# Optimization experiments

Measured on AMD Instinct MI355X. Metric: run time of the kernel, lower is better.

Reference implementation:

```python
import jax, jax.numpy as jnp
import numpy as np


def setup_inputs() -> dict:
    key = jax.random.key(0)
    ks = jax.random.split(key, 8)
    B, C, W, H = 4, 256, 64, 64
    Ck = C // 8  # 32, key/query channels
    x = jax.random.normal(ks[0], (B, C, W, H), dtype=jnp.float32)
    # 1x1 conv weights (xavier-uniform-like scale), biases zero per init_conv
    sf = (6.0 / (C + Ck)) ** 0.5
    sh = (6.0 / (C + C)) ** 0.5
    Wf = jax.random.uniform(ks[1], (Ck, C), jnp.float32, -sf, sf)
    Wg = jax.random.uniform(ks[2], (Ck, C), jnp.float32, -sf, sf)
    Wh = jax.random.uniform(ks[3], (C, C), jnp.float32, -sh, sh)
    bf = jnp.zeros((Ck,), jnp.float32)
    bg = jnp.zeros((Ck,), jnp.float32)
    bh = jnp.zeros((C,), jnp.float32)
    gamma = jax.random.uniform(ks[4], (1,), jnp.float32) * 0.5
    return {"x": x, "Wf": Wf, "bf": bf, "Wg": Wg, "bg": bg,
            "Wh": Wh, "bh": bh, "gamma": gamma}


def reference(x, Wf, bf, Wg, bg, Wh, bh, gamma):
    B, C, W, H = x.shape
    N = W * H
    xf = x.reshape(B, C, N)  # [B, C, N]
    # 1x1 convs == per-pixel linear maps
    f = jnp.einsum('kc,bcn->bkn', Wf, xf) + bf[None, :, None]  # [B, C/8, N]
    g = jnp.einsum('kc,bcn->bkn', Wg, xf) + bg[None, :, None]  # [B, C/8, N]
    h = jnp.einsum('oc,bcn->bon', Wh, xf) + bh[None, :, None]  # [B, C,   N]
    # attention[b, i, j] = sum_k f[b,k,i] * g[b,k,j]; softmax over j
    attn = jax.nn.softmax(jnp.einsum('bki,bkj->bij', f, g), axis=-1)  # [B,N,N]
    # bmm(h, attention): out[b,c,i] = sum_j h[b,c,j] * attn[b,j,i]
    sa = jnp.einsum('bcj,bji->bci', h, attn).reshape(B, C, W, H)
    return gamma[0] * sa + x
```

## Files before the change

### kernel.cpp

```cpp
#include <hip/hip_runtime.h>

#define NB 4
#define NC 256
#define NCK 32
#define NPIX 4096
#define TOT (NB * NC * NPIX)

typedef unsigned short u16;
typedef unsigned int u32;
typedef __bf16 bfv8 __attribute__((ext_vector_type(8)));
typedef float f32x4 __attribute__((ext_vector_type(4)));
#define LOG2E 1.4426950408889634f

__device__ inline u16 f2bf(float f) {
  union { float f; u32 u; } v; v.f = f;
  u32 r = v.u + 0x7fffu + ((v.u >> 16) & 1u);
  return (u16)(r >> 16);
}
__device__ inline float bf2f(u16 h) {
  union { u32 u; float f; } v; v.u = (u32)h << 16; return v.f;
}
__device__ inline u32 cvtpk(float a, float b) {
  u32 r;
  asm("v_cvt_pk_bf16_f32 %0, %1, %2" : "=v"(r) : "v"(a), "v"(b));
  return r;
}

__global__ __launch_bounds__(256) void k_fg(const float* __restrict__ x,
                                            const float* __restrict__ Wf,
                                            const float* __restrict__ bf_,
                                            const float* __restrict__ Wg,
                                            const float* __restrict__ bg_,
                                            u16* __restrict__ fP,
                                            u16* __restrict__ gT,
                                            u16* __restrict__ xT) {
  __shared__ float Wt[256][65];
  __shared__ float xl[32][68];
  __shared__ float tb[64][68];
  int blk = blockIdx.x;
  int b = blk >> 6;
  int n0 = (blk & 63) * 64;
  int t = threadIdx.x;
  int tx = t & 15, ty = t >> 4;
  for (int r = 0; r < 64; r++) {
    float w = (r < 32) ? Wf[r * 256 + t] : Wg[(r - 32) * 256 + t];
    Wt[t][r] = w;
  }
  float acc[4][4] = {};
  int n = t >> 2, cp = t & 3;
  for (int kc = 0; kc < 8; kc++) {
    __syncthreads();
#pragma unroll
    for (int r = 0; r < 2; r++) {
      int e = (r * 256 + t) * 4;
      int row = e >> 6, col = e & 63;
      *(float4*)&xl[row][col] =
          *(const float4*)(x + ((size_t)(b * NC + kc * 32 + row)) * NPIX + n0 + col);
    }
    __syncthreads();
    {
      u32 uu[4];
#pragma unroll
      for (int q = 0; q < 4; q++)
        uu[q] = cvtpk(xl[cp * 8 + 2 * q][n], xl[cp * 8 + 2 * q + 1][n]);
      *(uint4*)(xT + ((size_t)(b * NPIX) + n0 + n) * NC + kc * 32 + cp * 8) =
          make_uint4(uu[0], uu[1], uu[2], uu[3]);
    }
#pragma unroll
    for (int kk = 0; kk < 32; kk++) {
      float4 xv = *(const float4*)&xl[kk][tx * 4];
      float w0 = Wt[kc * 32 + kk][ty * 4 + 0];
      float w1 = Wt[kc * 32 + kk][ty * 4 + 1];
      float w2 = Wt[kc * 32 + kk][ty * 4 + 2];
      float w3 = Wt[kc * 32 + kk][ty * 4 + 3];
      acc[0][0] += w0 * xv.x; acc[0][1] += w0 * xv.y; acc[0][2] += w0 * xv.z; acc[0][3] += w0 * xv.w;
      acc[1][0] += w1 * xv.x; acc[1][1] += w1 * xv.y; acc[1][2] += w1 * xv.z; acc[1][3] += w1 * xv.w;
      acc[2][0] += w2 * xv.x; acc[2][1] += w2 * xv.y; acc[2][2] += w2 * xv.z; acc[2][3] += w2 * xv.w;
      acc[3][0] += w3 * xv.x; acc[3][1] += w3 * xv.y; acc[3][2] += w3 * xv.z; acc[3][3] += w3 * xv.w;
    }
  }
#pragma unroll
  for (int j = 0; j < 4; j++) {
    int o = ty * 4 + j;
    float bias = (o < 32) ? bf_[o] : bg_[o - 32];
#pragma unroll
    for (int vi = 0; vi < 4; vi++) tb[tx * 4 + vi][o] = acc[j][vi] + bias;
  }
  __syncthreads();
  int part = t & 3;
  {
    u32 ph[4], plo[4];
#pragma unroll
    for (int e = 0; e < 4; e++) {
      float v0 = tb[n][part * 8 + 2 * e + 0];
      float v1 = tb[n][part * 8 + 2 * e + 1];
      u16 h0 = f2bf(v0), h1 = f2bf(v1);
      u16 l0 = f2bf(v0 - bf2f(h0)), l1 = f2bf(v1 - bf2f(h1));
      ph[e] = (u32)h0 | ((u32)h1 << 16);
      plo[e] = (u32)l0 | ((u32)l1 << 16);
    }
    int jt_g = (n0 >> 4) + (n >> 4), r = n & 15;
    u16* dst = fP + ((size_t)(b * 256) + jt_g) * 1024 + r * 32 + part * 8;
    *(uint4*)dst = make_uint4(ph[0], ph[1], ph[2], ph[3]);
    *(uint4*)(dst + 512) = make_uint4(plo[0], plo[1], plo[2], plo[3]);
  }
  {
    u32 ph[4], plo[4];
#pragma unroll
    for (int e = 0; e < 4; e++) {
      float v0 = tb[n][32 + part * 8 + 2 * e + 0];
      float v1 = tb[n][32 + part * 8 + 2 * e + 1];
      u16 h0 = f2bf(v0), h1 = f2bf(v1);
      u16 l0 = f2bf(v0 - bf2f(h0)), l1 = f2bf(v1 - bf2f(h1));
      ph[e] = (u32)h0 | ((u32)h1 << 16);
      plo[e] = (u32)l0 | ((u32)l1 << 16);
    }
    u16* dst = gT + ((size_t)(b * NPIX) + n0 + n) * 64 + part * 8;
    *(uint4*)dst = make_uint4(ph[0], ph[1], ph[2], ph[3]);
    *(uint4*)(dst + 32) = make_uint4(plo[0], plo[1], plo[2], plo[3]);
  }
}

__global__ __launch_bounds__(256) void k_h(const u16* __restrict__ xT,
                                           const float* __restrict__ Wh,
                                           const float* __restrict__ bh,
                                           u16* __restrict__ h2) {
  __shared__ u16 At[128 * 32];
  __shared__ u16 Bt[128 * 32];
  int blk = blockIdx.x;
  int b = blk >> 6, r = blk & 63;
  int nt = r >> 1, ot = r & 1;
  int n0 = nt * 128, o0 = ot * 128;
  int t = threadIdx.x, lane = t & 63, w = t >> 6;
  int wr = w >> 1, wc = w & 1;
  int coll = lane & 15, cg = lane >> 4;
  f32x4 acc[4][4] = {};
  for (int kc = 0; kc < 8; kc++) {
    __syncthreads();
#pragma unroll
    for (int r2 = 0; r2 < 2; r2++) {
      int s = r2 * 256 + t;
      int row = s >> 2, slot = s & 3;
      int sw = (row ^ (row >> 2)) & 3;
      uint4 va = *(const uint4*)(xT + ((size_t)(b * NPIX + n0 + row)) * NC + kc * 32 + slot * 8);
      *(uint4*)((char*)At + row * 64 + ((slot ^ sw) * 16)) = va;
      const float* wsrc = Wh + (size_t)(o0 + row) * NC + kc * 32 + slot * 8;
      float4 w0 = *(const float4*)wsrc;
      float4 w1 = *(const float4*)(wsrc + 4);
      uint4 vb = make_uint4(cvtpk(w0.x, w0.y), cvtpk(w0.z, w0.w),
                            cvtpk(w1.x, w1.y), cvtpk(w1.z, w1.w));
      *(uint4*)((char*)Bt + row * 64 + ((slot ^ sw) * 16)) = vb;
    }
    __syncthreads();
    bfv8 af[4], bfr[4];
#pragma unroll
    for (int mi = 0; mi < 4; mi++) {
      int row = wr * 64 + mi * 16 + coll;
      int slot = cg ^ ((row ^ (row >> 2)) & 3);
      af[mi] = *(const bfv8*)((const char*)At + row * 64 + slot * 16);
    }
#pragma unroll
    for (int ni = 0; ni < 4; ni++) {
      int row = wc * 64 + ni * 16 + coll;
      int slot = cg ^ ((row ^ (row >> 2)) & 3);
      bfr[ni] = *(const bfv8*)((const char*)Bt + row * 64 + slot * 16);
    }
#pragma unroll
    for (int mi = 0; mi < 4; mi++)
#pragma unroll
      for (int ni = 0; ni < 4; ni++)
        acc[mi][ni] = __builtin_amdgcn_mfma_f32_16x16x32_bf16(af[mi], bfr[ni], acc[mi][ni], 0, 0, 0);
  }
#pragma unroll
  for (int ni = 0; ni < 4; ni++) {
    int o = o0 + wc * 64 + ni * 16 + coll;
    float bias = bh[o];
#pragma unroll
    for (int mi = 0; mi < 4; mi++) {
      int px = n0 + wr * 64 + mi * 16 + cg * 4;
      u32 lo = cvtpk(acc[mi][ni][0] + bias, acc[mi][ni][1] + bias);
      u32 hi = cvtpk(acc[mi][ni][2] + bias, acc[mi][ni][3] + bias);
      *(uint2*)(h2 + (((size_t)(b * 128) + (px >> 5)) * NC + o) * 32 + (px & 31)) =
          make_uint2(lo, hi);
    }
  }
}

__global__ __launch_bounds__(256) void k_pass1(const u16* __restrict__ fP,
                                               const u16* __restrict__ gT,
                                               float2* __restrict__ pmd) {
  __shared__ u16 gs[64 * 64];
  int blk = blockIdx.x;
  int iq = blk & 7, jt = (blk >> 3) & 63, b = blk >> 9;
  int j0 = jt * 64, ibase = iq * 512;
  int t = threadIdx.x, lane = t & 63, w = t >> 6;
  int coll = lane & 15, cg = lane >> 4;
  const u16* fr = fP + ((size_t)(b * 256) + (j0 >> 4) + w) * 1024 + coll * 32 + cg * 8;
  bfv8 ah = *(const bfv8*)fr;
  bfv8 al = *(const bfv8*)(fr + 512);
  float m[4] = {-3e38f, -3e38f, -3e38f, -3e38f}, d[4] = {0.f, 0.f, 0.f, 0.f};
  int r0 = t >> 3, s0 = t & 7;
  uint4 v0 = *(const uint4*)(gT + ((size_t)(b * NPIX) + ibase + r0) * 64 + s0 * 8);
  uint4 v1 = *(const uint4*)(gT + ((size_t)(b * NPIX) + ibase + 32 + r0) * 64 + s0 * 8);
  for (int it2 = 0; it2 < 8; ++it2) {
    __syncthreads();
    *(uint4*)(&gs[r0 * 64 + ((s0 ^ (r0 & 7)) << 3)]) = v0;
    *(uint4*)(&gs[(32 + r0) * 64 + ((s0 ^ (r0 & 7)) << 3)]) = v1;
    __syncthreads();
    if (it2 < 7) {
      v0 = *(const uint4*)(gT + ((size_t)(b * NPIX) + ibase + (it2 + 1) * 64 + r0) * 64 + s0 * 8);
      v1 = *(const uint4*)(gT + ((size_t)(b * NPIX) + ibase + (it2 + 1) * 64 + 32 + r0) * 64 + s0 * 8);
    }
    float sv[4][4];
#pragma unroll
    for (int t4 = 0; t4 < 4; ++t4) {
      int row = t4 * 16 + coll;
      const u16* base = &gs[row * 64];
      bfv8 bh = *(const bfv8*)(base + ((cg ^ (row & 7)) << 3));
      bfv8 bl = *(const bfv8*)(base + (((4 + cg) ^ (row & 7)) << 3));
      f32x4 s = {0.f, 0.f, 0.f, 0.f};
      s = __builtin_amdgcn_mfma_f32_16x16x32_bf16(al, bh, s, 0, 0, 0);
      s = __builtin_amdgcn_mfma_f32_16x16x32_bf16(ah, bl, s, 0, 0, 0);
      s = __builtin_amdgcn_mfma_f32_16x16x32_bf16(ah, bh, s, 0, 0, 0);
      sv[t4][0] = s[0]; sv[t4][1] = s[1]; sv[t4][2] = s[2]; sv[t4][3] = s[3];
    }
#pragma unroll
    for (int r = 0; r < 4; ++r) {
      float ms = fmaxf(fmaxf(sv[0][r], sv[1][r]), fmaxf(sv[2][r], sv[3][r]));
      float nm = fmaxf(m[r], ms);
      d[r] = d[r] * __expf(m[r] - nm) + __expf(sv[0][r] - nm) + __expf(sv[1][r] - nm) +
             __expf(sv[2][r] - nm) + __expf(sv[3][r] - nm);
      m[r] = nm;
    }
  }
#pragma unroll
  for (int r = 0; r < 4; ++r) {
#pragma unroll
    for (int off = 1; off < 16; off <<= 1) {
      float m2 = __shfl_xor(m[r], off);
      float d2 = __shfl_xor(d[r], off);
      float nm = fmaxf(m[r], m2);
      d[r] = d[r] * __expf(m[r] - nm) + d2 * __expf(m2 - nm);
      m[r] = nm;
    }
  }
  if (coll == 0) {
#pragma unroll
    for (int r = 0; r < 4; ++r) {
      int j = j0 + w * 16 + cg * 4 + r;
      pmd[((size_t)(b * 8 + iq)) * NPIX + j] = make_float2(m[r], d[r]);
    }
  }
}

__global__ __launch_bounds__(256) void k_comb(const float2* __restrict__ pmd,
                                              float* __restrict__ aout) {
  int idx = blockIdx.x * 256 + threadIdx.x;
  int b = idx >> 12, j = idx & 4095;
  float2 p[8];
  float M = -3e38f;
#pragma unroll
  for (int q = 0; q < 8; ++q) {
    p[q] = pmd[((size_t)(b * 8 + q)) * NPIX + j];
    M = fmaxf(M, p[q].x);
  }
  float D = 0.f;
#pragma unroll
  for (int q = 0; q < 8; ++q) D += p[q].y * __expf(p[q].x - M);
  aout[idx] = fmaf(M, LOG2E, __log2f(D));
}

__global__ __launch_bounds__(256, 2) void k_pass2(const u16* __restrict__ fP,
                                                  const u16* __restrict__ gT,
                                                  const u16* __restrict__ h2,
                                                  const float* __restrict__ arow,
                                                  u16* __restrict__ Opart) {
  __shared__ char smem[17408];
  int blk = blockIdx.x;
  int jq = blk & 1, it = (blk >> 1) & 63, b = blk >> 7;
  int i0 = it * 64, jbase = jq * 2048;
  int t = threadIdx.x, lane = t & 63, w = t >> 6;
  int coll = lane & 15, cg = lane >> 4;
  int cbase = w * 64;
  int swz = (coll & 7) << 4;
  const u16* gr = gT + ((size_t)(b * NPIX) + i0 + w * 16 + coll) * 64 + cg * 8;
  bfv8 gh = *(const bfv8*)gr;
  bfv8 gl = *(const bfv8*)(gr + 32);
  f32x4 acc[4][4] = {};
  const u16* h2b = h2 + (((size_t)(b * 128) + (jbase >> 5)) * NC + cbase + coll) * 32 + cg * 8;
  bfv8 hv[4][2];
#pragma unroll
  for (int ct = 0; ct < 4; ++ct)
#pragma unroll
    for (int kb = 0; kb < 2; ++kb)
      hv[ct][kb] = *(const bfv8*)(h2b + (size_t)kb * 8192 + ct * 512);
  const u16* fPb = fP + ((size_t)(b * 256) + (jbase >> 4)) * 1024 + coll * 32 + cg * 8;
  bfv8 fh[4], fl[4];
#pragma unroll
  for (int jt2 = 0; jt2 < 4; ++jt2) {
    fh[jt2] = *(const bfv8*)(fPb + jt2 * 1024);
    fl[jt2] = *(const bfv8*)(fPb + jt2 * 1024 + 512);
  }
  float apre = 0.f;
  if (t < 64) ((float*)(smem + 16384))[t] = arow[b * NPIX + jbase + t];
  f32x4 s[4];
#pragma unroll
  for (int jt2 = 0; jt2 < 4; ++jt2) {
    f32x4 ss = {0.f, 0.f, 0.f, 0.f};
    ss = __builtin_amdgcn_mfma_f32_16x16x32_bf16(fl[jt2], gh, ss, 0, 0, 0);
    ss = __builtin_amdgcn_mfma_f32_16x16x32_bf16(fh[jt2], gl, ss, 0, 0, 0);
    ss = __builtin_amdgcn_mfma_f32_16x16x32_bf16(fh[jt2], gh, ss, 0, 0, 0);
    s[jt2] = ss;
  }
#pragma unroll
  for (int jt2 = 0; jt2 < 4; ++jt2) {
    fh[jt2] = *(const bfv8*)(fPb + (4 + jt2) * 1024);
    fl[jt2] = *(const bfv8*)(fPb + (4 + jt2) * 1024 + 512);
  }
  if (t < 64) apre = arow[b * NPIX + jbase + 64 + t];
  __syncthreads();

  for (int jc = 0; jc < 32; ++jc) {
    int p = jc & 1;
    const float* alds = (const float*)(smem + 16384) + p * 64;
#pragma unroll
    for (int jt2 = 0; jt2 < 4; ++jt2) {
      int jr = jt2 * 16 + cg * 4;
      float4 av = *(const float4*)&alds[jr];
      float p0 = exp2f(fmaf(s[jt2][0], LOG2E, -av.x));
      float p1 = exp2f(fmaf(s[jt2][1], LOG2E, -av.y));
      float p2 = exp2f(fmaf(s[jt2][2], LOG2E, -av.z));
      float p3 = exp2f(fmaf(s[jt2][3], LOG2E, -av.w));
      char* pb = smem + p * 8192 + w * 2048 + coll * 128;
      *(uint2*)(pb + ((jt2 * 32 + cg * 8) ^ swz)) =
          make_uint2(cvtpk(p0, p1), cvtpk(p2, p3));
    }
    if (t < 64) ((float*)(smem + 16384))[((jc + 1) & 1) * 64 + t] = apre;
    __syncthreads();
#pragma unroll
    for (int ni = 0; ni < 4; ++ni) {
      const char* pbr = smem + p * 8192 + ni * 2048 + coll * 128;
      bfv8 pa0 = *(const bfv8*)(pbr + ((cg * 16) ^ swz));
      bfv8 pa1 = *(const bfv8*)(pbr + ((64 + cg * 16) ^ swz));
#pragma unroll
      for (int ct = 0; ct < 4; ++ct) {
        acc[ct][ni] = __builtin_amdgcn_mfma_f32_16x16x32_bf16(hv[ct][0], pa0, acc[ct][ni], 0, 0, 0);
        acc[ct][ni] = __builtin_amdgcn_mfma_f32_16x16x32_bf16(hv[ct][1], pa1, acc[ct][ni], 0, 0, 0);
      }
    }
    if (jc < 31) {
#pragma unroll
      for (int ct = 0; ct < 4; ++ct)
#pragma unroll
        for (int kb = 0; kb < 2; ++kb)
          hv[ct][kb] =
              *(const bfv8*)(h2b + (size_t)((jc + 1) * 2 + kb) * 8192 + ct * 512);
#pragma unroll
      for (int jt2 = 0; jt2 < 4; ++jt2) {
        f32x4 ss = {0.f, 0.f, 0.f, 0.f};
        ss = __builtin_amdgcn_mfma_f32_16x16x32_bf16(fl[jt2], gh, ss, 0, 0, 0);
        ss = __builtin_amdgcn_mfma_f32_16x16x32_bf16(fh[jt2], gl, ss, 0, 0, 0);
        ss = __builtin_amdgcn_mfma_f32_16x16x32_bf16(fh[jt2], gh, ss, 0, 0, 0);
        s[jt2] = ss;
      }
      if (jc < 30) {
#pragma unroll
        for (int jt2 = 0; jt2 < 4; ++jt2) {
          fh[jt2] = *(const bfv8*)(fPb + (size_t)((jc + 2) * 4 + jt2) * 1024);
          fl[jt2] = *(const bfv8*)(fPb + (size_t)((jc + 2) * 4 + jt2) * 1024 + 512);
        }
        if (t < 64) apre = arow[b * NPIX + jbase + (jc + 2) * 64 + t];
      }
    }
  }
  int rr = lane >> 2, part = lane & 3;
  for (int rd = 0; rd < 4; ++rd) {
    __syncthreads();
    float* tbf = (float*)smem;
#pragma unroll
    for (int ni = 0; ni < 4; ++ni)
#pragma unroll
      for (int r = 0; r < 4; ++r)
        tbf[(w * 16 + cg * 4 + r) * 68 + ni * 16 + coll] = acc[rd][ni][r];
    __syncthreads();
    const float* src = &((float*)smem)[(w * 16 + rr) * 68 + part * 16];
    u32 uu[8];
#pragma unroll
    for (int q = 0; q < 8; ++q) uu[q] = cvtpk(src[2 * q], src[2 * q + 1]);
    u16* op = Opart + (size_t)jq * TOT +
              ((size_t)(b * NC) + cbase + rd * 16 + rr) * NPIX + i0 + part * 16;
    *(uint4*)op = make_uint4(uu[0], uu[1], uu[2], uu[3]);
    *(uint4*)(op + 8) = make_uint4(uu[4], uu[5], uu[6], uu[7]);
  }
}

__global__ __launch_bounds__(256) void k_reduce(const u16* __restrict__ Opart,
                                                const float* __restrict__ x,
                                                const float* __restrict__ gamma,
                                                float* __restrict__ out) {
  int i = (blockIdx.x * 256 + threadIdx.x) * 4;
  uint2 a = *(const uint2*)(Opart + i);
  uint2 c = *(const uint2*)(Opart + TOT + i);
  float4 xv = *(const float4*)(x + i);
  float gam = gamma[0];
  float4 ov;
  ov.x = gam * (bf2f((u16)(a.x & 0xffff)) + bf2f((u16)(c.x & 0xffff))) + xv.x;
  ov.y = gam * (bf2f((u16)(a.x >> 16)) + bf2f((u16)(c.x >> 16))) + xv.y;
  ov.z = gam * (bf2f((u16)(a.y & 0xffff)) + bf2f((u16)(c.y & 0xffff))) + xv.z;
  ov.w = gam * (bf2f((u16)(a.y >> 16)) + bf2f((u16)(c.y >> 16))) + xv.w;
  *(float4*)(out + i) = ov;
}

extern "C" void kernel_launch(void* const* d_in, const int* in_sizes, int n_in,
                              void* d_out, int out_size, void* d_ws, size_t ws_size,
                              hipStream_t stream) {
  (void)in_sizes; (void)n_in; (void)out_size; (void)ws_size;
  const float* x = (const float*)d_in[0];
  const float* Wf = (const float*)d_in[1];
  const float* bf_ = (const float*)d_in[2];
  const float* Wg = (const float*)d_in[3];
  const float* bg_ = (const float*)d_in[4];
  const float* Wh = (const float*)d_in[5];
  const float* bh = (const float*)d_in[6];
  const float* gamma = (const float*)d_in[7];
  float* out = (float*)d_out;
  char* ws = (char*)d_ws;
  const size_t M1 = 1u << 20;
  u16* xT = (u16*)ws;
  u16* Opart = (u16*)ws;
  u16* h2 = (u16*)(ws + 17 * M1);
  u16* fP = (u16*)(ws + 25 * M1);
  u16* gT = (u16*)(ws + 27 * M1);
  float* aout = (float*)(ws + 29 * M1);
  float2* pmd = (float2*)(ws + 29 * M1 + (1u << 17));

  k_fg<<<256, 256, 0, stream>>>(x, Wf, bf_, Wg, bg_, fP, gT, xT);
  k_pass1<<<2048, 256, 0, stream>>>(fP, gT, pmd);
  k_h<<<256, 256, 0, stream>>>(xT, Wh, bh, h2);
  k_comb<<<64, 256, 0, stream>>>(pmd, aout);
  k_pass2<<<512, 256, 0, stream>>>(fP, gT, h2, aout, Opart);
  k_reduce<<<4096, 256, 0, stream>>>(Opart, x, gamma, out);
}
```

Measured before the change: 136.0 us.

## Double-buffer h registers and reschedule pass2 loop with priority hints

Unrolls the pass2 main loop by two and double-buffers the h operand registers (hvA/hvB), so the h load for chunk jc+2 is issued a full iteration ahead instead of right after use. The QK^T score MFMAs are moved ahead of the PV MFMAs, and s_setprio raises wave priority around MFMA bursts. The __syncthreads is replaced with a custom barrier that only waits on LDS counters and fences scheduling, so global prefetches stay in flight across it. Loads are now unconditional with clamped indices, which removes branches but adds register pressure under the two-waves-per-SIMD launch bound.

```diff
diff --git a/kernel.cpp b/kernel.cpp
--- a/kernel.cpp
+++ b/kernel.cpp
@@ -24,6 +24,13 @@
   u32 r;
   asm("v_cvt_pk_bf16_f32 %0, %1, %2" : "=v"(r) : "v"(a), "v"(b));
   return r;
+}
+__device__ inline void bar_lds() {
+  __builtin_amdgcn_sched_barrier(0);
+  asm volatile("s_waitcnt lgkmcnt(0)" ::: "memory");
+  __builtin_amdgcn_s_barrier();
+  asm volatile("" ::: "memory");
+  __builtin_amdgcn_sched_barrier(0);
 }
 
 __global__ __launch_bounds__(256) void k_fg(const float* __restrict__ x,
@@ -270,6 +277,56 @@
   aout[idx] = fmaf(M, LOG2E, __log2f(D));
 }
 
+#define PASS2_BODY(JC, P, HC)                                                            \
+  {                                                                                      \
+    const int jc = (JC);                                                                 \
+    const float* alds = (const float*)(smem + 16384) + (P) * 64;                         \
+    _Pragma("unroll") for (int jt2 = 0; jt2 < 4; ++jt2) {                                \
+      int jr = jt2 * 16 + cg * 4;                                                        \
+      float4 av = *(const float4*)&alds[jr];                                             \
+      float p0 = exp2f(fmaf(s[jt2][0], LOG2E, -av.x));                                   \
+      float p1 = exp2f(fmaf(s[jt2][1], LOG2E, -av.y));                                   \
+      float p2 = exp2f(fmaf(s[jt2][2], LOG2E, -av.z));                                   \
+      float p3 = exp2f(fmaf(s[jt2][3], LOG2E, -av.w));                                   \
+      char* pb = smem + (P) * 8192 + w * 2048 + coll * 128;                              \
+      *(uint2*)(pb + ((jt2 * 32 + cg * 8) ^ swz)) =                                      \
+          make_uint2(cvtpk(p0, p1), cvtpk(p2, p3));                                      \
+    }                                                                                    \
+    if (t < 64) ((float*)(smem + 16384))[(1 - (P)) * 64 + t] = apre;                     \
+    bar_lds();                                                                           \
+    int jn = (jc + 2 <= 31) ? jc + 2 : 31;                                               \
+    __builtin_amdgcn_s_setprio(1);                                                       \
+    _Pragma("unroll") for (int jt2 = 0; jt2 < 4; ++jt2) {                                \
+      f32x4 ss = {0.f, 0.f, 0.f, 0.f};                                                   \
+      ss = __builtin_amdgcn_mfma_f32_16x16x32_bf16(fl[jt2], gh, ss, 0, 0, 0);            \
+      ss = __builtin_amdgcn_mfma_f32_16x16x32_bf16(fh[jt2], gl, ss, 0, 0, 0);            \
+      ss = __builtin_amdgcn_mfma_f32_16x16x32_bf16(fh[jt2], gh, ss, 0, 0, 0);            \
+      s[jt2] = ss;                                                                       \
+    }                                                                                    \
+    __builtin_amdgcn_s_setprio(0);                                                       \
+    _Pragma("unroll") for (int jt2 = 0; jt2 < 4; ++jt2) {                                \
+      fh[jt2] = *(const bfv8*)(fPb + (size_t)(jn * 4 + jt2) * 1024);                     \
+      fl[jt2] = *(const bfv8*)(fPb + (size_t)(jn * 4 + jt2) * 1024 + 512);               \
+    }                                                                                    \
+    apre = arow[b * NPIX + jbase + jn * 64 + (t & 63)];                                  \
+    __builtin_amdgcn_s_setprio(1);                                                       \
+    _Pragma("unroll") for (int ni = 0; ni < 4; ++ni) {                                   \
+      const char* pbr = smem + (P) * 8192 + ni * 2048 + coll * 128;                      \
+      bfv8 pa0 = *(const bfv8*)(pbr + ((cg * 16) ^ swz));                                \
+      bfv8 pa1 = *(const bfv8*)(pbr + ((64 + cg * 16) ^ swz));                           \
+      _Pragma("unroll") for (int ct = 0; ct < 4; ++ct) {                                 \
+        acc[ct][ni] = __builtin_amdgcn_mfma_f32_16x16x32_bf16(HC[ct][0], pa0,            \
+                                                              acc[ct][ni], 0, 0, 0);    \
+        acc[ct][ni] = __builtin_amdgcn_mfma_f32_16x16x32_bf16(HC[ct][1], pa1,            \
+                                                              acc[ct][ni], 0, 0, 0);    \
+      }                                                                                  \
+    }                                                                                    \
+    __builtin_amdgcn_s_setprio(0);                                                       \
+    _Pragma("unroll") for (int ct = 0; ct < 4; ++ct)                                     \
+      _Pragma("unroll") for (int kb = 0; kb < 2; ++kb)                                   \
+        HC[ct][kb] = *(const bfv8*)(h2b + (size_t)(jn * 2 + kb) * 8192 + ct * 512);      \
+  }
+
 __global__ __launch_bounds__(256, 2) void k_pass2(const u16* __restrict__ fP,
                                                   const u16* __restrict__ gT,
                                                   const u16* __restrict__ h2,
@@ -288,21 +345,23 @@
   bfv8 gl = *(const bfv8*)(gr + 32);
   f32x4 acc[4][4] = {};
   const u16* h2b = h2 + (((size_t)(b * 128) + (jbase >> 5)) * NC + cbase + coll) * 32 + cg * 8;
-  bfv8 hv[4][2];
+  const u16* fPb = fP + ((size_t)(b * 256) + (jbase >> 4)) * 1024 + coll * 32 + cg * 8;
+  bfv8 hvA[4][2], hvB[4][2];
 #pragma unroll
   for (int ct = 0; ct < 4; ++ct)
 #pragma unroll
-    for (int kb = 0; kb < 2; ++kb)
-      hv[ct][kb] = *(const bfv8*)(h2b + (size_t)kb * 8192 + ct * 512);
-  const u16* fPb = fP + ((size_t)(b * 256) + (jbase >> 4)) * 1024 + coll * 32 + cg * 8;
+    for (int kb = 0; kb < 2; ++kb) {
+      hvA[ct][kb] = *(const bfv8*)(h2b + (size_t)kb * 8192 + ct * 512);
+      hvB[ct][kb] = *(const bfv8*)(h2b + (size_t)(2 + kb) * 8192 + ct * 512);
+    }
   bfv8 fh[4], fl[4];
 #pragma unroll
   for (int jt2 = 0; jt2 < 4; ++jt2) {
     fh[jt2] = *(const bfv8*)(fPb + jt2 * 1024);
     fl[jt2] = *(const bfv8*)(fPb + jt2 * 1024 + 512);
   }
-  float apre = 0.f;
   if (t < 64) ((float*)(smem + 16384))[t] = arow[b * NPIX + jbase + t];
+  float apre = arow[b * NPIX + jbase + 64 + (t & 63)];
   f32x4 s[4];
 #pragma unroll
   for (int jt2 = 0; jt2 < 4; ++jt2) {
@@ -317,61 +376,10 @@
     fh[jt2] = *(const bfv8*)(fPb + (4 + jt2) * 1024);
     fl[jt2] = *(const bfv8*)(fPb + (4 + jt2) * 1024 + 512);
   }
-  if (t < 64) apre = arow[b * NPIX + jbase + 64 + t];
   __syncthreads();
-
-  for (int jc = 0; jc < 32; ++jc) {
-    int p = jc & 1;
-    const float* alds = (const float*)(smem + 16384) + p * 64;
-#pragma unroll
-    for (int jt2 = 0; jt2 < 4; ++jt2) {
-      int jr = jt2 * 16 + cg * 4;
-      float4 av = *(const float4*)&alds[jr];
-      float p0 = exp2f(fmaf(s[jt2][0], LOG2E, -av.x));
-      float p1 = exp2f(fmaf(s[jt2][1], LOG2E, -av.y));
-      float p2 = exp2f(fmaf(s[jt2][2], LOG2E, -av.z));
-      float p3 = exp2f(fmaf(s[jt2][3], LOG2E, -av.w));
-      char* pb = smem + p * 8192 + w * 2048 + coll * 128;
-      *(uint2*)(pb + ((jt2 * 32 + cg * 8) ^ swz)) =
-          make_uint2(cvtpk(p0, p1), cvtpk(p2, p3));
-    }
-    if (t < 64) ((float*)(smem + 16384))[((jc + 1) & 1) * 64 + t] = apre;
-    __syncthreads();
-#pragma unroll
-    for (int ni = 0; ni < 4; ++ni) {
-      const char* pbr = smem + p * 8192 + ni * 2048 + coll * 128;
-      bfv8 pa0 = *(const bfv8*)(pbr + ((cg * 16) ^ swz));
-      bfv8 pa1 = *(const bfv8*)(pbr + ((64 + cg * 16) ^ swz));
-#pragma unroll
-      for (int ct = 0; ct < 4; ++ct) {
-        acc[ct][ni] = __builtin_amdgcn_mfma_f32_16x16x32_bf16(hv[ct][0], pa0, acc[ct][ni], 0, 0, 0);
-        acc[ct][ni] = __builtin_amdgcn_mfma_f32_16x16x32_bf16(hv[ct][1], pa1, acc[ct][ni], 0, 0, 0);
-      }
-    }
-    if (jc < 31) {
-#pragma unroll
-      for (int ct = 0; ct < 4; ++ct)
-#pragma unroll
-        for (int kb = 0; kb < 2; ++kb)
-          hv[ct][kb] =
-              *(const bfv8*)(h2b + (size_t)((jc + 1) * 2 + kb) * 8192 + ct * 512);
-#pragma unroll
-      for (int jt2 = 0; jt2 < 4; ++jt2) {
-        f32x4 ss = {0.f, 0.f, 0.f, 0.f};
-        ss = __builtin_amdgcn_mfma_f32_16x16x32_bf16(fl[jt2], gh, ss, 0, 0, 0);
-        ss = __builtin_amdgcn_mfma_f32_16x16x32_bf16(fh[jt2], gl, ss, 0, 0, 0);
-        ss = __builtin_amdgcn_mfma_f32_16x16x32_bf16(fh[jt2], gh, ss, 0, 0, 0);
-        s[jt2] = ss;
-      }
-      if (jc < 30) {
-#pragma unroll
-        for (int jt2 = 0; jt2 < 4; ++jt2) {
-          fh[jt2] = *(const bfv8*)(fPb + (size_t)((jc + 2) * 4 + jt2) * 1024);
-          fl[jt2] = *(const bfv8*)(fPb + (size_t)((jc + 2) * 4 + jt2) * 1024 + 512);
-        }
-        if (t < 64) apre = arow[b * NPIX + jbase + (jc + 2) * 64 + t];
-      }
-    }
+  for (int jc2 = 0; jc2 < 16; ++jc2) {
+    PASS2_BODY(2 * jc2, 0, hvA)
+    PASS2_BODY(2 * jc2 + 1, 1, hvB)
   }
   int rr = lane >> 2, part = lane & 3;
   for (int rd = 0; rd < 4; ++rd) {
```

Measured after the change: 139.1 us. 1.02x slower.

## Halve pass2 i-tile to 32 pixels, doubling blocks and raising occupancy

Applied to the files above, without the earlier changes.

The attention-apply kernel now tiles 32 query pixels per block instead of 64, so twice as many blocks are launched. Each wave computes scores for a quarter of the j-chunk and one i half, and accumulator and LDS footprints shrink, allowing launch_bounds of 4 blocks per CU. The aim is better latency hiding and more parallelism across CUs. In exchange the h tiles are reloaded by twice as many blocks, which raises global and L2 traffic per output.

```diff
diff --git a/kernel.cpp b/kernel.cpp
--- a/kernel.cpp
+++ b/kernel.cpp
@@ -270,23 +270,25 @@
   aout[idx] = fmaf(M, LOG2E, __log2f(D));
 }
 
-__global__ __launch_bounds__(256, 2) void k_pass2(const u16* __restrict__ fP,
+__global__ __launch_bounds__(256, 4) void k_pass2(const u16* __restrict__ fP,
                                                   const u16* __restrict__ gT,
                                                   const u16* __restrict__ h2,
                                                   const float* __restrict__ arow,
                                                   u16* __restrict__ Opart) {
-  __shared__ char smem[17408];
+  __shared__ char smem[10240];
   int blk = blockIdx.x;
-  int jq = blk & 1, it = (blk >> 1) & 63, b = blk >> 7;
-  int i0 = it * 64, jbase = jq * 2048;
+  int jq = blk & 1, it = (blk >> 1) & 127, b = blk >> 8;
+  int i0 = it * 32, jbase = jq * 2048;
   int t = threadIdx.x, lane = t & 63, w = t >> 6;
   int coll = lane & 15, cg = lane >> 4;
+  int isub = w & 1, jp = w >> 1;
   int cbase = w * 64;
   int swz = (coll & 7) << 4;
-  const u16* gr = gT + ((size_t)(b * NPIX) + i0 + w * 16 + coll) * 64 + cg * 8;
+  float* alds = (float*)(smem + 8192);
+  const u16* gr = gT + ((size_t)(b * NPIX) + i0 + isub * 16 + coll) * 64 + cg * 8;
   bfv8 gh = *(const bfv8*)gr;
   bfv8 gl = *(const bfv8*)(gr + 32);
-  f32x4 acc[4][4] = {};
+  f32x4 acc[4][2] = {};
   const u16* h2b = h2 + (((size_t)(b * 128) + (jbase >> 5)) * NC + cbase + coll) * 32 + cg * 8;
   bfv8 hv[4][2];
 #pragma unroll
@@ -295,51 +297,51 @@
     for (int kb = 0; kb < 2; ++kb)
       hv[ct][kb] = *(const bfv8*)(h2b + (size_t)kb * 8192 + ct * 512);
   const u16* fPb = fP + ((size_t)(b * 256) + (jbase >> 4)) * 1024 + coll * 32 + cg * 8;
-  bfv8 fh[4], fl[4];
-#pragma unroll
-  for (int jt2 = 0; jt2 < 4; ++jt2) {
-    fh[jt2] = *(const bfv8*)(fPb + jt2 * 1024);
-    fl[jt2] = *(const bfv8*)(fPb + jt2 * 1024 + 512);
+  bfv8 fh[2], fl[2];
+#pragma unroll
+  for (int q = 0; q < 2; ++q) {
+    fh[q] = *(const bfv8*)(fPb + (jp * 2 + q) * 1024);
+    fl[q] = *(const bfv8*)(fPb + (jp * 2 + q) * 1024 + 512);
   }
   float apre = 0.f;
-  if (t < 64) ((float*)(smem + 16384))[t] = arow[b * NPIX + jbase + t];
-  f32x4 s[4];
-#pragma unroll
-  for (int jt2 = 0; jt2 < 4; ++jt2) {
+  if (t < 64) alds[t] = arow[b * NPIX + jbase + t];
+  f32x4 s[2];
+#pragma unroll
+  for (int q = 0; q < 2; ++q) {
     f32x4 ss = {0.f, 0.f, 0.f, 0.f};
-    ss = __builtin_amdgcn_mfma_f32_16x16x32_bf16(fl[jt2], gh, ss, 0, 0, 0);
-    ss = __builtin_amdgcn_mfma_f32_16x16x32_bf16(fh[jt2], gl, ss, 0, 0, 0);
-    ss = __builtin_amdgcn_mfma_f32_16x16x32_bf16(fh[jt2], gh, ss, 0, 0, 0);
-    s[jt2] = ss;
-  }
-#pragma unroll
-  for (int jt2 = 0; jt2 < 4; ++jt2) {
-    fh[jt2] = *(const bfv8*)(fPb + (4 + jt2) * 1024);
-    fl[jt2] = *(const bfv8*)(fPb + (4 + jt2) * 1024 + 512);
+    ss = __builtin_amdgcn_mfma_f32_16x16x32_bf16(fl[q], gh, ss, 0, 0, 0);
+    ss = __builtin_amdgcn_mfma_f32_16x16x32_bf16(fh[q], gl, ss, 0, 0, 0);
+    ss = __builtin_amdgcn_mfma_f32_16x16x32_bf16(fh[q], gh, ss, 0, 0, 0);
+    s[q] = ss;
+  }
+#pragma unroll
+  for (int q = 0; q < 2; ++q) {
+    fh[q] = *(const bfv8*)(fPb + (4 + jp * 2 + q) * 1024);
+    fl[q] = *(const bfv8*)(fPb + (4 + jp * 2 + q) * 1024 + 512);
   }
   if (t < 64) apre = arow[b * NPIX + jbase + 64 + t];
   __syncthreads();
 
   for (int jc = 0; jc < 32; ++jc) {
     int p = jc & 1;
-    const float* alds = (const float*)(smem + 16384) + p * 64;
-#pragma unroll
-    for (int jt2 = 0; jt2 < 4; ++jt2) {
-      int jr = jt2 * 16 + cg * 4;
-      float4 av = *(const float4*)&alds[jr];
-      float p0 = exp2f(fmaf(s[jt2][0], LOG2E, -av.x));
-      float p1 = exp2f(fmaf(s[jt2][1], LOG2E, -av.y));
-      float p2 = exp2f(fmaf(s[jt2][2], LOG2E, -av.z));
-      float p3 = exp2f(fmaf(s[jt2][3], LOG2E, -av.w));
-      char* pb = smem + p * 8192 + w * 2048 + coll * 128;
-      *(uint2*)(pb + ((jt2 * 32 + cg * 8) ^ swz)) =
+#pragma unroll
+    for (int q = 0; q < 2; ++q) {
+      int jtl = jp * 2 + q;
+      int jr = jtl * 16 + cg * 4;
+      float4 av = *(const float4*)&alds[p * 64 + jr];
+      float p0 = exp2f(fmaf(s[q][0], LOG2E, -av.x));
+      float p1 = exp2f(fmaf(s[q][1], LOG2E, -av.y));
+      float p2 = exp2f(fmaf(s[q][2], LOG2E, -av.z));
+      float p3 = exp2f(fmaf(s[q][3], LOG2E, -av.w));
+      char* pb = smem + p * 4096 + isub * 2048 + coll * 128;
+      *(uint2*)(pb + ((jtl * 32 + cg * 8) ^ swz)) =
           make_uint2(cvtpk(p0, p1), cvtpk(p2, p3));
     }
-    if (t < 64) ((float*)(smem + 16384))[((jc + 1) & 1) * 64 + t] = apre;
-    __syncthreads();
-#pragma unroll
-    for (int ni = 0; ni < 4; ++ni) {
-      const char* pbr = smem + p * 8192 + ni * 2048 + coll * 128;
+    if (t < 64) alds[((jc + 1) & 1) * 64 + t] = apre;
+    __syncthreads();
+#pragma unroll
+    for (int ni = 0; ni < 2; ++ni) {
+      const char* pbr = smem + p * 4096 + ni * 2048 + coll * 128;
       bfv8 pa0 = *(const bfv8*)(pbr + ((cg * 16) ^ swz));
       bfv8 pa1 = *(const bfv8*)(pbr + ((64 + cg * 16) ^ swz));
 #pragma unroll
@@ -353,44 +355,42 @@
       for (int ct = 0; ct < 4; ++ct)
 #pragma unroll
         for (int kb = 0; kb < 2; ++kb)
-          hv[ct][kb] =
-              *(const bfv8*)(h2b + (size_t)((jc + 1) * 2 + kb) * 8192 + ct * 512);
-#pragma unroll
-      for (int jt2 = 0; jt2 < 4; ++jt2) {
+          hv[ct][kb] = *(const bfv8*)(h2b + (size_t)((jc + 1) * 2 + kb) * 8192 + ct * 512);
+#pragma unroll
+      for (int q = 0; q < 2; ++q) {
         f32x4 ss = {0.f, 0.f, 0.f, 0.f};
-        ss = __builtin_amdgcn_mfma_f32_16x16x32_bf16(fl[jt2], gh, ss, 0, 0, 0);
-        ss = __builtin_amdgcn_mfma_f32_16x16x32_bf16(fh[jt2], gl, ss, 0, 0, 0);
-        ss = __builtin_amdgcn_mfma_f32_16x16x32_bf16(fh[jt2], gh, ss, 0, 0, 0);
-        s[jt2] = ss;
+        ss = __builtin_amdgcn_mfma_f32_16x16x32_bf16(fl[q], gh, ss, 0, 0, 0);
+        ss = __builtin_amdgcn_mfma_f32_16x16x32_bf16(fh[q], gl, ss, 0, 0, 0);
+        ss = __builtin_amdgcn_mfma_f32_16x16x32_bf16(fh[q], gh, ss, 0, 0, 0);
+        s[q] = ss;
       }
       if (jc < 30) {
 #pragma unroll
-        for (int jt2 = 0; jt2 < 4; ++jt2) {
-          fh[jt2] = *(const bfv8*)(fPb + (size_t)((jc + 2) * 4 + jt2) * 1024);
-          fl[jt2] = *(const bfv8*)(fPb + (size_t)((jc + 2) * 4 + jt2) * 1024 + 512);
+        for (int q = 0; q < 2; ++q) {
+          fh[q] = *(const bfv8*)(fPb + (size_t)((jc + 2) * 4 + jp * 2 + q) * 1024);
+          fl[q] = *(const bfv8*)(fPb + (size_t)((jc + 2) * 4 + jp * 2 + q) * 1024 + 512);
         }
         if (t < 64) apre = arow[b * NPIX + jbase + (jc + 2) * 64 + t];
       }
     }
   }
-  int rr = lane >> 2, part = lane & 3;
+  int row = lane >> 2, part = lane & 3;
   for (int rd = 0; rd < 4; ++rd) {
     __syncthreads();
-    float* tbf = (float*)smem;
-#pragma unroll
-    for (int ni = 0; ni < 4; ++ni)
+    float* tbf = (float*)(smem + w * 2304);
+#pragma unroll
+    for (int ni = 0; ni < 2; ++ni)
 #pragma unroll
       for (int r = 0; r < 4; ++r)
-        tbf[(w * 16 + cg * 4 + r) * 68 + ni * 16 + coll] = acc[rd][ni][r];
-    __syncthreads();
-    const float* src = &((float*)smem)[(w * 16 + rr) * 68 + part * 16];
-    u32 uu[8];
-#pragma unroll
-    for (int q = 0; q < 8; ++q) uu[q] = cvtpk(src[2 * q], src[2 * q + 1]);
+        tbf[(cg * 4 + r) * 36 + ni * 16 + coll] = acc[rd][ni][r];
+    __syncthreads();
+    const float* src = tbf + row * 36 + part * 8;
+    u32 uu[4];
+#pragma unroll
+    for (int q = 0; q < 4; ++q) uu[q] = cvtpk(src[2 * q], src[2 * q + 1]);
     u16* op = Opart + (size_t)jq * TOT +
-              ((size_t)(b * NC) + cbase + rd * 16 + rr) * NPIX + i0 + part * 16;
+              ((size_t)(b * NC) + cbase + rd * 16 + row) * NPIX + i0 + part * 8;
     *(uint4*)op = make_uint4(uu[0], uu[1], uu[2], uu[3]);
-    *(uint4*)(op + 8) = make_uint4(uu[4], uu[5], uu[6], uu[7]);
   }
 }
 
@@ -438,6 +438,6 @@
   k_pass1<<<2048, 256, 0, stream>>>(fP, gT, pmd);
   k_h<<<256, 256, 0, stream>>>(xT, Wh, bh, h2);
   k_comb<<<64, 256, 0, stream>>>(pmd, aout);
-  k_pass2<<<512, 256, 0, stream>>>(fP, gT, h2, aout, Opart);
+  k_pass2<<<1024, 256, 0, stream>>>(fP, gT, h2, aout, Opart);
   k_reduce<<<4096, 256, 0, stream>>>(Opart, x, gamma, out);
 }
```

After: 163.1 us. 1.2x slower.
